# Optimization experiments

Hardware: AMD Instinct MI355X
Metric: run time of the kernel (lower is better)

The kernel has to match this reference:

```python
import jax, jax.numpy as jnp
import numpy as np

CODE_SIZE = 8
NUM_HEADS = 16
KC = 2 ** CODE_SIZE  # 256 codebook buckets


def setup_inputs() -> dict:
    key = jax.random.key(0)
    ks = jax.random.split(key, 6)
    B, Lq, Lk, C = 8, 2048, 4096, 1024
    q = jax.random.normal(ks[0], (B * Lq, C), jnp.float32)
    k = jax.random.normal(ks[1], (B * Lk, C), jnp.float32)
    v = jax.random.normal(ks[2], (B * Lk, C), jnp.float32)
    Wc = jax.random.normal(ks[3], (CODE_SIZE, C), jnp.float32) * (C ** -0.5)  # code_proj weight
    bc = jnp.zeros((CODE_SIZE,), jnp.float32)                                  # code_proj bias
    codebook = jax.random.normal(ks[4], (2 * CODE_SIZE, C), jnp.float32) * 0.02
    lengths = jnp.full((B,), Lk, jnp.int32)      # kv tokens per sample
    inv_lengths = jnp.full((B,), Lq, jnp.int32)  # q tokens per sample
    return dict(q=q, k=k, v=v, Wc=Wc, bc=bc, codebook=codebook,
                lengths=lengths, inv_lengths=inv_lengths)


def reference(q, k, v, Wc, bc, codebook, lengths, inv_lengths):
    C = q.shape[-1]
    d = C // NUM_HEADS
    scale = d ** -0.5
    B = lengths.shape[0]
    Lk = k.shape[0] // B  # equal per-sample kv lengths
    Lq = q.shape[0] // B  # equal per-sample q lengths

    # --- binary spherical quantization of k ---
    code = k @ Wc.T + bc
    code = code / jnp.linalg.norm(code, axis=-1, keepdims=True)
    # sign in {-1,+1}/sqrt(cs); affine *sqrt(cs)/2 + 0.5 -> bits in {0,1}
    bits = (code >= 0).astype(jnp.int32)                      # [B*Lk, cs]
    code_base = 2 ** jnp.arange(CODE_SIZE - 1, -1, -1)        # [cs]
    idxs = (bits * code_base).sum(-1)                         # [B*Lk] in [0, 256)

    # --- dense codebook keys for all 2^cs codes ---
    base_bits = (jnp.arange(KC)[:, None] // code_base) % 2    # [K, cs]
    base = jnp.concatenate([base_bits, 1 - base_bits], axis=-1).astype(codebook.dtype)  # [K, 2cs]
    cod_k = base @ codebook                                   # [K, C]

    # --- scatter-add v and counts into per-sample buckets ---
    b_idx = jnp.repeat(jnp.arange(B), Lk)                     # batch id per kv token
    flat = b_idx * KC + idxs                                  # [B*Lk]
    cod_v = jax.ops.segment_sum(v, flat, num_segments=B * KC).reshape(B, KC, C)
    counts = jax.ops.segment_sum(jnp.ones((B * Lk,), q.dtype), flat,
                                 num_segments=B * KC).reshape(B, KC)

    # --- bucketed attention with quotient normalization ---
    qh = q.reshape(B, Lq, NUM_HEADS, d)
    kh = cod_k.reshape(KC, NUM_HEADS, d)
    vh = cod_v.reshape(B, KC, NUM_HEADS, d)
    scores = scale * jnp.einsum('blhd,khd->blhk', qh, kh)     # [B,Lq,H,K]
    bias = jnp.where(counts > 0, 0.0, -jnp.inf)[:, None, None, :]  # mask empty buckets
    attn = jax.nn.softmax(scores + bias, axis=-1)
    num = jnp.einsum('blhk,bkhd->blhd', attn, vh)             # attn @ summed-v
    den = jnp.einsum('blhk,bk->blh', attn, counts)            # attn @ counts
    out = num / den[..., None]
    return out.reshape(B * Lq, C)
```

## Files before the change

kernel.cpp:

```cpp
#include <hip/hip_runtime.h>
#include <hip/hip_bf16.h>

constexpr int B  = 8;
constexpr int LQ = 2048;
constexpr int LK = 4096;
constexpr int C  = 1024;
constexpr int H  = 16;
constexpr int D  = 64;
constexpr int CS = 8;
constexpr int KC = 256;
constexpr float SCALE = 0.125f;

typedef __attribute__((ext_vector_type(8))) short short8;
typedef __attribute__((ext_vector_type(4))) float f32x4;

union FragU { unsigned u[4]; short8 s; float4 f; };

__device__ inline unsigned bfp(float a, float b) {
  float2 f2; f2.x = a; f2.y = b;
  __hip_bfloat162 h = __float22bfloat162_rn(f2);
  return *reinterpret_cast<unsigned*>(&h);
}
__device__ inline unsigned short bf1(float a) {
  __hip_bfloat16 h = __float2bfloat16(a);
  return *reinterpret_cast<unsigned short*>(&h);
}

__global__ __launch_bounds__(256) void k_codes(
    const float* __restrict__ kmat, const float* __restrict__ Wc,
    const float* __restrict__ bc, int* __restrict__ idx)
{
  __shared__ float wS[CS * C];
  const int tid = threadIdx.x;
  {
    const float4* wsrc = (const float4*)Wc;
    float4* wdst = (float4*)wS;
#pragma unroll
    for (int i = 0; i < 8; ++i) wdst[tid + i * 256] = wsrc[tid + i * 256];
  }
  float bcr[CS];
#pragma unroll
  for (int j = 0; j < CS; ++j) bcr[j] = bc[j];
  __syncthreads();

  const int wave = tid >> 6, lane = tid & 63;

  for (int i = 0; i < 8; ++i) {
    const int r = blockIdx.x * 32 + wave * 8 + i;
    const float4* krow = (const float4*)(kmat + (size_t)r * C);
    float acc[CS];
#pragma unroll
    for (int j = 0; j < CS; ++j) acc[j] = 0.f;
#pragma unroll
    for (int rep = 0; rep < 4; ++rep) {
      float4 kv = krow[rep * 64 + lane];
      const int dbase = (rep * 64 + lane) * 4;
#pragma unroll
      for (int j = 0; j < CS; ++j) {
        float4 wv = *(const float4*)&wS[j * C + dbase];
        acc[j] += kv.x * wv.x + kv.y * wv.y + kv.z * wv.z + kv.w * wv.w;
      }
    }
#pragma unroll
    for (int j = 0; j < CS; ++j) {
#pragma unroll
      for (int off = 32; off >= 1; off >>= 1)
        acc[j] += __shfl_xor(acc[j], off, 64);
    }
    if (lane == 0) {
      int ix = 0;
#pragma unroll
      for (int j = 0; j < CS; ++j)
        ix |= ((acc[j] + bcr[j]) >= 0.f ? 1 : 0) << (7 - j);
      idx[r] = ix;
    }
  }
}

__global__ __launch_bounds__(256) void k_sort(
    const int* __restrict__ idx, int* __restrict__ offs,
    int* __restrict__ cnti, int* __restrict__ perm,
    float4* __restrict__ vfc)
{
  __shared__ int idxS[LK];
  __shared__ int hist[KC];
  __shared__ int cur[KC];
  __shared__ int wsum[4];
  const int b = blockIdx.x, t = threadIdx.x;
  const int lane = t & 63, w = t >> 6;

  hist[t] = 0;
  __syncthreads();
  for (int i = t; i < LK; i += 256) {
    const int ix = idx[b * LK + i];
    idxS[i] = ix;
    atomicAdd(&hist[ix], 1);
  }
  __syncthreads();

  const int myc = hist[t];
  int scan = myc;
#pragma unroll
  for (int off = 1; off < 64; off <<= 1) {
    int u = __shfl_up(scan, off, 64);
    if (lane >= off) scan += u;
  }
  if (lane == 63) wsum[w] = scan;
  __syncthreads();
  int base = 0;
#pragma unroll
  for (int i = 0; i < 4; ++i) base += (i < w) ? wsum[i] : 0;
  const int start = b * LK + base + scan - myc;
  offs[b * KC + t] = start;
  cnti[b * KC + t] = myc;
  cur[t] = start;
  __syncthreads();

  for (int i = t; i < LK; i += 256) {
    const int pos = atomicAdd(&cur[idxS[i]], 1);
    perm[pos] = b * LK + i;
  }

  for (int i = t; i < 512; i += 256) {
    const int qc = i >> 6, ln = i & 63;
    FragU u4;
    if ((ln & 15) == 0) {
      const int* cs = hist + (qc * 4 + (ln >> 4)) * 8;
      u4.u[0] = bfp((float)cs[0], (float)cs[1]);
      u4.u[1] = bfp((float)cs[2], (float)cs[3]);
      u4.u[2] = bfp((float)cs[4], (float)cs[5]);
      u4.u[3] = bfp((float)cs[6], (float)cs[7]);
    } else {
      u4.u[0] = u4.u[1] = u4.u[2] = u4.u[3] = 0u;
    }
    vfc[b * 512 + i] = u4.f;
  }
}

__global__ __launch_bounds__(256) void k_gather(
    const float* __restrict__ v, const int* __restrict__ perm,
    const int* __restrict__ offs, const int* __restrict__ cnti,
    unsigned short* __restrict__ vbf)
{
  __shared__ int permS[512];
  const int t = threadIdx.x;
  const int ix = blockIdx.x, b = blockIdx.y;
  const int start = offs[b * KC + ix];
  const int cnt = cnti[b * KC + ix];

  float4 acc = make_float4(0.f, 0.f, 0.f, 0.f);
  for (int base = 0; base < cnt; base += 512) {
    const int n = min(512, cnt - base);
    __syncthreads();
    for (int i = t; i < n; i += 256) permS[i] = perm[start + base + i];
    __syncthreads();
    int i = 0;
    for (; i + 4 <= n; i += 4) {
      const int r0 = permS[i], r1 = permS[i + 1];
      const int r2 = permS[i + 2], r3 = permS[i + 3];
      float4 a = *(const float4*)(v + (size_t)r0 * C + t * 4);
      float4 b4 = *(const float4*)(v + (size_t)r1 * C + t * 4);
      float4 c4 = *(const float4*)(v + (size_t)r2 * C + t * 4);
      float4 d4 = *(const float4*)(v + (size_t)r3 * C + t * 4);
      acc.x += a.x + b4.x + c4.x + d4.x;
      acc.y += a.y + b4.y + c4.y + d4.y;
      acc.z += a.z + b4.z + c4.z + d4.z;
      acc.w += a.w + b4.w + c4.w + d4.w;
    }
    for (; i < n; ++i) {
      const int r0 = permS[i];
      float4 a = *(const float4*)(v + (size_t)r0 * C + t * 4);
      acc.x += a.x; acc.y += a.y; acc.z += a.z; acc.w += a.w;
    }
  }

  const int h = t >> 4;
  const int n0 = (t & 15) * 4;
  const int o = ix >> 3, r = ix & 7;
  const int slot0 = ((o >> 2) * 4 + (n0 >> 4)) * 64 + (o & 3) * 16 + (n0 & 15);
  unsigned short* dst = vbf + ((size_t)((b * 16 + h) * 2048 + slot0)) * 8 + r;
  dst[0]  = bf1(acc.x);
  dst[8]  = bf1(acc.y);
  dst[16] = bf1(acc.z);
  dst[24] = bf1(acc.w);
}

__global__ __launch_bounds__(256) void k_attn(
    const float* __restrict__ q, const float* __restrict__ cb,
    const float4* __restrict__ vfb, const float4* __restrict__ vfc,
    float* __restrict__ out)
{
  __shared__ __align__(16) char smem[18432];
  float4* QA  = (float4*)smem;
  float4* CBf = (float4*)(smem + 16384);
  float*  TS  = (float*)smem;

  const int tid = threadIdx.x;
  const int lane = tid & 63, wq = tid >> 6, quad = lane >> 4;
  const int h = blockIdx.y, b = blockIdx.z;
  const int q0 = blockIdx.x * 128;

#pragma unroll
  for (int it = 0; it < 4; ++it) {
    const int od = tid & 7, m = it * 32 + (tid >> 3);
    const float* src = q + (size_t)(b * LQ + q0 + m) * C + h * D + od * 8;
    float4 f0 = *(const float4*)src, f1 = *(const float4*)(src + 4);
    FragU u;
    u.u[0] = bfp(f0.x * SCALE, f0.y * SCALE);
    u.u[1] = bfp(f0.z * SCALE, f0.w * SCALE);
    u.u[2] = bfp(f1.x * SCALE, f1.y * SCALE);
    u.u[3] = bfp(f1.z * SCALE, f1.w * SCALE);
    QA[((m >> 4) * 2 + (od >> 2)) * 64 + (od & 3) * 16 + (m & 15)] = u.f;
  }
  if (tid < 128) {
    const int od = tid & 7, j = tid >> 3;
    const float* src = cb + (size_t)j * C + h * D + od * 8;
    float4 f0 = *(const float4*)src, f1 = *(const float4*)(src + 4);
    FragU u;
    u.u[0] = bfp(f0.x, f0.y); u.u[1] = bfp(f0.z, f0.w);
    u.u[2] = bfp(f1.x, f1.y); u.u[3] = bfp(f1.z, f1.w);
    CBf[(od >> 2) * 64 + (od & 3) * 16 + j] = u.f;
  }
  __syncthreads();

  f32x4 tacc[2];
#pragma unroll
  for (int mt2 = 0; mt2 < 2; ++mt2) {
    const int mt = wq * 2 + mt2;
    FragU a0, a1, b0, b1;
    a0.f = QA[(mt * 2 + 0) * 64 + lane];
    a1.f = QA[(mt * 2 + 1) * 64 + lane];
    b0.f = CBf[0 * 64 + lane];
    b1.f = CBf[1 * 64 + lane];
    f32x4 z = {0.f, 0.f, 0.f, 0.f};
    z = __builtin_amdgcn_mfma_f32_16x16x32_bf16(a0.s, b0.s, z, 0, 0, 0);
    z = __builtin_amdgcn_mfma_f32_16x16x32_bf16(a1.s, b1.s, z, 0, 0, 0);
    tacc[mt2] = z;
  }
  __syncthreads();

#pragma unroll
  for (int mt2 = 0; mt2 < 2; ++mt2) {
    const int mt = wq * 2 + mt2;
#pragma unroll
    for (int r = 0; r < 4; ++r)
      TS[mt * 272 + (quad * 4 + r) * 17 + (lane & 15)] = tacc[mt2][r];
  }
  float t0[16], t1[16];
#pragma unroll
  for (int j = 0; j < 16; ++j) {
    t0[j] = TS[(wq * 2 + 0) * 272 + (lane & 15) * 17 + j];
    t1[j] = TS[(wq * 2 + 1) * 272 + (lane & 15) * 17 + j];
  }

  float esl0[8], esl1[8];
#pragma unroll
  for (int c = 0; c < 8; ++c) {
    esl0[c] = __expf(((c & 4) ? t0[5] : t0[13]) + ((c & 2) ? t0[6] : t0[14]) +
                     ((c & 1) ? t0[7] : t0[15]));
    esl1[c] = __expf(((c & 4) ? t1[5] : t1[13]) + ((c & 2) ? t1[6] : t1[14]) +
                     ((c & 1) ? t1[7] : t1[15]));
  }

  f32x4 acc[2][5];
#pragma unroll
  for (int i = 0; i < 2; ++i)
#pragma unroll
    for (int t_ = 0; t_ < 5; ++t_) acc[i][t_] = (f32x4){0.f, 0.f, 0.f, 0.f};

  const float4* vb = vfb + (size_t)(b * 16 + h) * 2048 + lane;
  const float4* vc = vfc + b * 512 + lane;

#pragma unroll
  for (int qc = 0; qc < 8; ++qc) {
    FragU bf0, bf1_, bf2, bf3, cf;
    bf0.f = vb[(qc * 4 + 0) * 64];
    bf1_.f = vb[(qc * 4 + 1) * 64];
    bf2.f = vb[(qc * 4 + 2) * 64];
    bf3.f = vb[(qc * 4 + 3) * 64];
    cf.f  = vc[qc * 64];

    const int u = qc * 4 + quad;
    const float eshi0 = __expf(
        ((u & 16) ? t0[0] : t0[8]) + ((u & 8) ? t0[1] : t0[9]) +
        ((u & 4) ? t0[2] : t0[10]) + ((u & 2) ? t0[3] : t0[11]) +
        ((u & 1) ? t0[4] : t0[12]));
    const float eshi1 = __expf(
        ((u & 16) ? t1[0] : t1[8]) + ((u & 8) ? t1[1] : t1[9]) +
        ((u & 4) ? t1[2] : t1[10]) + ((u & 2) ? t1[3] : t1[11]) +
        ((u & 1) ? t1[4] : t1[12]));

    FragU a0, a1;
    a0.u[0] = bfp(eshi0 * esl0[0], eshi0 * esl0[1]);
    a0.u[1] = bfp(eshi0 * esl0[2], eshi0 * esl0[3]);
    a0.u[2] = bfp(eshi0 * esl0[4], eshi0 * esl0[5]);
    a0.u[3] = bfp(eshi0 * esl0[6], eshi0 * esl0[7]);
    a1.u[0] = bfp(eshi1 * esl1[0], eshi1 * esl1[1]);
    a1.u[1] = bfp(eshi1 * esl1[2], eshi1 * esl1[3]);
    a1.u[2] = bfp(eshi1 * esl1[4], eshi1 * esl1[5]);
    a1.u[3] = bfp(eshi1 * esl1[6], eshi1 * esl1[7]);

    acc[0][0] = __builtin_amdgcn_mfma_f32_16x16x32_bf16(a0.s, bf0.s,  acc[0][0], 0, 0, 0);
    acc[1][0] = __builtin_amdgcn_mfma_f32_16x16x32_bf16(a1.s, bf0.s,  acc[1][0], 0, 0, 0);
    acc[0][1] = __builtin_amdgcn_mfma_f32_16x16x32_bf16(a0.s, bf1_.s, acc[0][1], 0, 0, 0);
    acc[1][1] = __builtin_amdgcn_mfma_f32_16x16x32_bf16(a1.s, bf1_.s, acc[1][1], 0, 0, 0);
    acc[0][2] = __builtin_amdgcn_mfma_f32_16x16x32_bf16(a0.s, bf2.s,  acc[0][2], 0, 0, 0);
    acc[1][2] = __builtin_amdgcn_mfma_f32_16x16x32_bf16(a1.s, bf2.s,  acc[1][2], 0, 0, 0);
    acc[0][3] = __builtin_amdgcn_mfma_f32_16x16x32_bf16(a0.s, bf3.s,  acc[0][3], 0, 0, 0);
    acc[1][3] = __builtin_amdgcn_mfma_f32_16x16x32_bf16(a1.s, bf3.s,  acc[1][3], 0, 0, 0);
    acc[0][4] = __builtin_amdgcn_mfma_f32_16x16x32_bf16(a0.s, cf.s,   acc[0][4], 0, 0, 0);
    acc[1][4] = __builtin_amdgcn_mfma_f32_16x16x32_bf16(a1.s, cf.s,   acc[1][4], 0, 0, 0);
  }

  const int srcl = lane & 48;
#pragma unroll
  for (int mt2 = 0; mt2 < 2; ++mt2) {
#pragma unroll
    for (int r = 0; r < 4; ++r) {
      const float den = __shfl(acc[mt2][4][r], srcl, 64);
      const float inv = 1.0f / den;
      const int row = q0 + wq * 32 + mt2 * 16 + quad * 4 + r;
      float* op = out + (size_t)(b * LQ + row) * C + h * D + (lane & 15);
#pragma unroll
      for (int t_ = 0; t_ < 4; ++t_) op[t_ * 16] = acc[mt2][t_][r] * inv;
    }
  }
}

extern "C" void kernel_launch(void* const* d_in, const int* in_sizes, int n_in,
                              void* d_out, int out_size, void* d_ws, size_t ws_size,
                              hipStream_t stream) {
  (void)in_sizes; (void)n_in; (void)out_size; (void)ws_size;
  const float* q  = (const float*)d_in[0];
  const float* k  = (const float*)d_in[1];
  const float* v  = (const float*)d_in[2];
  const float* Wc = (const float*)d_in[3];
  const float* bc = (const float*)d_in[4];
  const float* cb = (const float*)d_in[5];
  float* out = (float*)d_out;

  char* ws = (char*)d_ws;
  int*    idxp  = (int*)ws;
  int*    offsp = (int*)(ws + 0x20000);
  int*    cntip = (int*)(ws + 0x22000);
  int*    permp = (int*)(ws + 0x24000);
  float4* vfcp  = (float4*)(ws + 0x44000);
  unsigned short* vbfp = (unsigned short*)(ws + 0x60000);

  hipLaunchKernelGGL(k_codes, dim3(1024), dim3(256), 0, stream,
                     k, Wc, bc, idxp);
  hipLaunchKernelGGL(k_sort, dim3(B), dim3(256), 0, stream,
                     idxp, offsp, cntip, permp, vfcp);
  hipLaunchKernelGGL(k_gather, dim3(KC, B), dim3(256), 0, stream,
                     v, permp, offsp, cntip, vbfp);
  hipLaunchKernelGGL(k_attn, dim3(LQ / 128, H, B), dim3(256), 0, stream,
                     q, cb, (const float4*)vbfp, (const float4*)vfcp, out);
}
```

Measured before the change: 376.9 us.

## Fuse four kernels into one persistent kernel with software grid barriers

Replaces the codes/sort/gather/attention kernel chain with a single persistent 512-block kernel separated by atomic-based grid barriers, plus a small init kernel. The histogram is built with global atomics during code computation, and the gather is retiled so each block handles 8 buckets over half the channels and writes packed bf16 fragments. Attention tiles are mapped so each XCD handles one batch, and outputs use nontemporal stores. This removes launch gaps and the tail of the serial 8-block sort. In exchange it relies on all 512 blocks being co-resident, only 8 blocks do the sort while the rest wait at a barrier, and a timeout in the spin loop could silently break correctness.

```diff
diff --git a/kernel.cpp b/kernel.cpp
--- a/kernel.cpp
+++ b/kernel.cpp
@@ -9,6 +9,7 @@
 constexpr int D  = 64;
 constexpr int CS = 8;
 constexpr int KC = 256;
+constexpr int GRID = 512;
 constexpr float SCALE = 0.125f;
 
 typedef __attribute__((ext_vector_type(8))) short short8;
@@ -21,308 +22,322 @@
   __hip_bfloat162 h = __float22bfloat162_rn(f2);
   return *reinterpret_cast<unsigned*>(&h);
 }
-__device__ inline unsigned short bf1(float a) {
-  __hip_bfloat16 h = __float2bfloat16(a);
-  return *reinterpret_cast<unsigned short*>(&h);
-}
-
-__global__ __launch_bounds__(256) void k_codes(
-    const float* __restrict__ kmat, const float* __restrict__ Wc,
-    const float* __restrict__ bc, int* __restrict__ idx)
+
+__device__ inline void gridbar(int* bar) {
+  __syncthreads();
+  if (threadIdx.x == 0) {
+    __threadfence();
+    const int g = __hip_atomic_load(bar + 1, __ATOMIC_RELAXED, __HIP_MEMORY_SCOPE_AGENT);
+    const int a = __hip_atomic_fetch_add(bar, 1, __ATOMIC_ACQ_REL, __HIP_MEMORY_SCOPE_AGENT);
+    if (a == GRID - 1) {
+      __hip_atomic_store(bar, 0, __ATOMIC_RELAXED, __HIP_MEMORY_SCOPE_AGENT);
+      __hip_atomic_fetch_add(bar + 1, 1, __ATOMIC_RELEASE, __HIP_MEMORY_SCOPE_AGENT);
+    } else {
+      int it = 0;
+      while (__hip_atomic_load(bar + 1, __ATOMIC_ACQUIRE, __HIP_MEMORY_SCOPE_AGENT) == g) {
+        if (++it > 2000000) break;
+        __builtin_amdgcn_s_sleep(8);
+      }
+    }
+    __threadfence();
+  }
+  __syncthreads();
+}
+
+__global__ __launch_bounds__(256) void k_init(int* __restrict__ histg,
+                                              int* __restrict__ bar)
 {
-  __shared__ float wS[CS * C];
+  const int i = blockIdx.x * 256 + threadIdx.x;
+  if (i < B * KC) histg[i] = 0;
+  if (i == 0) { bar[0] = 0; bar[1] = 0; }
+}
+
+__global__ __launch_bounds__(256, 2) void k_fused(
+    const float* __restrict__ q, const float* __restrict__ kmat,
+    const float* __restrict__ v, const float* __restrict__ Wc,
+    const float* __restrict__ bc, const float* __restrict__ cb,
+    float* __restrict__ out,
+    int* __restrict__ idx, int* __restrict__ histg,
+    int* __restrict__ offs, int* __restrict__ cnti, int* __restrict__ perm,
+    float4* __restrict__ vfc, float4* __restrict__ vfb,
+    int* __restrict__ bar)
+{
+  __shared__ __align__(16) char smem[32768];
   const int tid = threadIdx.x;
+  const int lane = tid & 63, wave = tid >> 6;
+
   {
+    float* wS = (float*)smem;
     const float4* wsrc = (const float4*)Wc;
     float4* wdst = (float4*)wS;
 #pragma unroll
     for (int i = 0; i < 8; ++i) wdst[tid + i * 256] = wsrc[tid + i * 256];
-  }
-  float bcr[CS];
-#pragma unroll
-  for (int j = 0; j < CS; ++j) bcr[j] = bc[j];
-  __syncthreads();
-
-  const int wave = tid >> 6, lane = tid & 63;
-
-  for (int i = 0; i < 8; ++i) {
-    const int r = blockIdx.x * 32 + wave * 8 + i;
-    const float4* krow = (const float4*)(kmat + (size_t)r * C);
-    float acc[CS];
-#pragma unroll
-    for (int j = 0; j < CS; ++j) acc[j] = 0.f;
-#pragma unroll
-    for (int rep = 0; rep < 4; ++rep) {
-      float4 kv = krow[rep * 64 + lane];
-      const int dbase = (rep * 64 + lane) * 4;
-#pragma unroll
-      for (int j = 0; j < CS; ++j) {
-        float4 wv = *(const float4*)&wS[j * C + dbase];
-        acc[j] += kv.x * wv.x + kv.y * wv.y + kv.z * wv.z + kv.w * wv.w;
-      }
-    }
-#pragma unroll
-    for (int j = 0; j < CS; ++j) {
-#pragma unroll
-      for (int off = 32; off >= 1; off >>= 1)
-        acc[j] += __shfl_xor(acc[j], off, 64);
-    }
-    if (lane == 0) {
-      int ix = 0;
-#pragma unroll
-      for (int j = 0; j < CS; ++j)
-        ix |= ((acc[j] + bcr[j]) >= 0.f ? 1 : 0) << (7 - j);
-      idx[r] = ix;
-    }
-  }
-}
-
-__global__ __launch_bounds__(256) void k_sort(
-    const int* __restrict__ idx, int* __restrict__ offs,
-    int* __restrict__ cnti, int* __restrict__ perm,
-    float4* __restrict__ vfc)
-{
-  __shared__ int idxS[LK];
-  __shared__ int hist[KC];
-  __shared__ int cur[KC];
-  __shared__ int wsum[4];
-  const int b = blockIdx.x, t = threadIdx.x;
-  const int lane = t & 63, w = t >> 6;
-
-  hist[t] = 0;
-  __syncthreads();
-  for (int i = t; i < LK; i += 256) {
-    const int ix = idx[b * LK + i];
-    idxS[i] = ix;
-    atomicAdd(&hist[ix], 1);
-  }
-  __syncthreads();
-
-  const int myc = hist[t];
-  int scan = myc;
-#pragma unroll
-  for (int off = 1; off < 64; off <<= 1) {
-    int u = __shfl_up(scan, off, 64);
-    if (lane >= off) scan += u;
-  }
-  if (lane == 63) wsum[w] = scan;
-  __syncthreads();
-  int base = 0;
-#pragma unroll
-  for (int i = 0; i < 4; ++i) base += (i < w) ? wsum[i] : 0;
-  const int start = b * LK + base + scan - myc;
-  offs[b * KC + t] = start;
-  cnti[b * KC + t] = myc;
-  cur[t] = start;
-  __syncthreads();
-
-  for (int i = t; i < LK; i += 256) {
-    const int pos = atomicAdd(&cur[idxS[i]], 1);
-    perm[pos] = b * LK + i;
-  }
-
-  for (int i = t; i < 512; i += 256) {
-    const int qc = i >> 6, ln = i & 63;
-    FragU u4;
-    if ((ln & 15) == 0) {
-      const int* cs = hist + (qc * 4 + (ln >> 4)) * 8;
-      u4.u[0] = bfp((float)cs[0], (float)cs[1]);
-      u4.u[1] = bfp((float)cs[2], (float)cs[3]);
-      u4.u[2] = bfp((float)cs[4], (float)cs[5]);
-      u4.u[3] = bfp((float)cs[6], (float)cs[7]);
-    } else {
-      u4.u[0] = u4.u[1] = u4.u[2] = u4.u[3] = 0u;
-    }
-    vfc[b * 512 + i] = u4.f;
-  }
-}
-
-__global__ __launch_bounds__(256) void k_gather(
-    const float* __restrict__ v, const int* __restrict__ perm,
-    const int* __restrict__ offs, const int* __restrict__ cnti,
-    unsigned short* __restrict__ vbf)
-{
-  __shared__ int permS[512];
-  const int t = threadIdx.x;
-  const int ix = blockIdx.x, b = blockIdx.y;
-  const int start = offs[b * KC + ix];
-  const int cnt = cnti[b * KC + ix];
-
-  float4 acc = make_float4(0.f, 0.f, 0.f, 0.f);
-  for (int base = 0; base < cnt; base += 512) {
-    const int n = min(512, cnt - base);
+    float bcr[CS];
+#pragma unroll
+    for (int j = 0; j < CS; ++j) bcr[j] = bc[j];
     __syncthreads();
-    for (int i = t; i < n; i += 256) permS[i] = perm[start + base + i];
+
+    for (int chunk = blockIdx.x; chunk < (B * LK) / 16; chunk += GRID) {
+      for (int i = 0; i < 4; ++i) {
+        const int r = chunk * 16 + wave * 4 + i;
+        const float4* krow = (const float4*)(kmat + (size_t)r * C);
+        float acc[CS];
+#pragma unroll
+        for (int j = 0; j < CS; ++j) acc[j] = 0.f;
+#pragma unroll
+        for (int rep = 0; rep < 4; ++rep) {
+          float4 kv = krow[rep * 64 + lane];
+          const int dbase = (rep * 64 + lane) * 4;
+#pragma unroll
+          for (int j = 0; j < CS; ++j) {
+            float4 wv = *(const float4*)&wS[j * C + dbase];
+            acc[j] += kv.x * wv.x + kv.y * wv.y + kv.z * wv.z + kv.w * wv.w;
+          }
+        }
+#pragma unroll
+        for (int j = 0; j < CS; ++j) {
+#pragma unroll
+          for (int off = 32; off >= 1; off >>= 1)
+            acc[j] += __shfl_xor(acc[j], off, 64);
+        }
+        if (lane == 0) {
+          int ix = 0;
+#pragma unroll
+          for (int j = 0; j < CS; ++j)
+            ix |= ((acc[j] + bcr[j]) >= 0.f ? 1 : 0) << (7 - j);
+          idx[r] = ix;
+          atomicAdd(&histg[(r >> 12) * KC + ix], 1);
+        }
+      }
+    }
+  }
+  gridbar(bar);
+
+  if (blockIdx.x < B) {
+    int* idxS = (int*)smem;
+    int* cur  = (int*)(smem + 16384);
+    int* wsum = (int*)(smem + 17408);
+    const int b = blockIdx.x;
+    for (int i = tid; i < LK; i += 256) idxS[i] = idx[b * LK + i];
+    const int myc = histg[b * KC + tid];
+    int scan = myc;
+#pragma unroll
+    for (int off = 1; off < 64; off <<= 1) {
+      int u = __shfl_up(scan, off, 64);
+      if (lane >= off) scan += u;
+    }
+    if (lane == 63) wsum[wave] = scan;
     __syncthreads();
-    int i = 0;
-    for (; i + 4 <= n; i += 4) {
-      const int r0 = permS[i], r1 = permS[i + 1];
-      const int r2 = permS[i + 2], r3 = permS[i + 3];
-      float4 a = *(const float4*)(v + (size_t)r0 * C + t * 4);
-      float4 b4 = *(const float4*)(v + (size_t)r1 * C + t * 4);
-      float4 c4 = *(const float4*)(v + (size_t)r2 * C + t * 4);
-      float4 d4 = *(const float4*)(v + (size_t)r3 * C + t * 4);
-      acc.x += a.x + b4.x + c4.x + d4.x;
-      acc.y += a.y + b4.y + c4.y + d4.y;
-      acc.z += a.z + b4.z + c4.z + d4.z;
-      acc.w += a.w + b4.w + c4.w + d4.w;
-    }
-    for (; i < n; ++i) {
-      const int r0 = permS[i];
-      float4 a = *(const float4*)(v + (size_t)r0 * C + t * 4);
-      acc.x += a.x; acc.y += a.y; acc.z += a.z; acc.w += a.w;
-    }
-  }
-
-  const int h = t >> 4;
-  const int n0 = (t & 15) * 4;
-  const int o = ix >> 3, r = ix & 7;
-  const int slot0 = ((o >> 2) * 4 + (n0 >> 4)) * 64 + (o & 3) * 16 + (n0 & 15);
-  unsigned short* dst = vbf + ((size_t)((b * 16 + h) * 2048 + slot0)) * 8 + r;
-  dst[0]  = bf1(acc.x);
-  dst[8]  = bf1(acc.y);
-  dst[16] = bf1(acc.z);
-  dst[24] = bf1(acc.w);
-}
-
-__global__ __launch_bounds__(256) void k_attn(
-    const float* __restrict__ q, const float* __restrict__ cb,
-    const float4* __restrict__ vfb, const float4* __restrict__ vfc,
-    float* __restrict__ out)
-{
-  __shared__ __align__(16) char smem[18432];
-  float4* QA  = (float4*)smem;
-  float4* CBf = (float4*)(smem + 16384);
-  float*  TS  = (float*)smem;
-
-  const int tid = threadIdx.x;
-  const int lane = tid & 63, wq = tid >> 6, quad = lane >> 4;
-  const int h = blockIdx.y, b = blockIdx.z;
-  const int q0 = blockIdx.x * 128;
-
-#pragma unroll
-  for (int it = 0; it < 4; ++it) {
-    const int od = tid & 7, m = it * 32 + (tid >> 3);
-    const float* src = q + (size_t)(b * LQ + q0 + m) * C + h * D + od * 8;
-    float4 f0 = *(const float4*)src, f1 = *(const float4*)(src + 4);
-    FragU u;
-    u.u[0] = bfp(f0.x * SCALE, f0.y * SCALE);
-    u.u[1] = bfp(f0.z * SCALE, f0.w * SCALE);
-    u.u[2] = bfp(f1.x * SCALE, f1.y * SCALE);
-    u.u[3] = bfp(f1.z * SCALE, f1.w * SCALE);
-    QA[((m >> 4) * 2 + (od >> 2)) * 64 + (od & 3) * 16 + (m & 15)] = u.f;
-  }
-  if (tid < 128) {
-    const int od = tid & 7, j = tid >> 3;
-    const float* src = cb + (size_t)j * C + h * D + od * 8;
-    float4 f0 = *(const float4*)src, f1 = *(const float4*)(src + 4);
-    FragU u;
-    u.u[0] = bfp(f0.x, f0.y); u.u[1] = bfp(f0.z, f0.w);
-    u.u[2] = bfp(f1.x, f1.y); u.u[3] = bfp(f1.z, f1.w);
-    CBf[(od >> 2) * 64 + (od & 3) * 16 + j] = u.f;
-  }
-  __syncthreads();
-
-  f32x4 tacc[2];
-#pragma unroll
-  for (int mt2 = 0; mt2 < 2; ++mt2) {
-    const int mt = wq * 2 + mt2;
-    FragU a0, a1, b0, b1;
-    a0.f = QA[(mt * 2 + 0) * 64 + lane];
-    a1.f = QA[(mt * 2 + 1) * 64 + lane];
-    b0.f = CBf[0 * 64 + lane];
-    b1.f = CBf[1 * 64 + lane];
-    f32x4 z = {0.f, 0.f, 0.f, 0.f};
-    z = __builtin_amdgcn_mfma_f32_16x16x32_bf16(a0.s, b0.s, z, 0, 0, 0);
-    z = __builtin_amdgcn_mfma_f32_16x16x32_bf16(a1.s, b1.s, z, 0, 0, 0);
-    tacc[mt2] = z;
-  }
-  __syncthreads();
-
-#pragma unroll
-  for (int mt2 = 0; mt2 < 2; ++mt2) {
-    const int mt = wq * 2 + mt2;
-#pragma unroll
-    for (int r = 0; r < 4; ++r)
-      TS[mt * 272 + (quad * 4 + r) * 17 + (lane & 15)] = tacc[mt2][r];
-  }
-  float t0[16], t1[16];
-#pragma unroll
-  for (int j = 0; j < 16; ++j) {
-    t0[j] = TS[(wq * 2 + 0) * 272 + (lane & 15) * 17 + j];
-    t1[j] = TS[(wq * 2 + 1) * 272 + (lane & 15) * 17 + j];
-  }
-
-  float esl0[8], esl1[8];
-#pragma unroll
-  for (int c = 0; c < 8; ++c) {
-    esl0[c] = __expf(((c & 4) ? t0[5] : t0[13]) + ((c & 2) ? t0[6] : t0[14]) +
-                     ((c & 1) ? t0[7] : t0[15]));
-    esl1[c] = __expf(((c & 4) ? t1[5] : t1[13]) + ((c & 2) ? t1[6] : t1[14]) +
-                     ((c & 1) ? t1[7] : t1[15]));
-  }
-
-  f32x4 acc[2][5];
-#pragma unroll
-  for (int i = 0; i < 2; ++i)
-#pragma unroll
-    for (int t_ = 0; t_ < 5; ++t_) acc[i][t_] = (f32x4){0.f, 0.f, 0.f, 0.f};
-
-  const float4* vb = vfb + (size_t)(b * 16 + h) * 2048 + lane;
-  const float4* vc = vfc + b * 512 + lane;
-
-#pragma unroll
-  for (int qc = 0; qc < 8; ++qc) {
-    FragU bf0, bf1_, bf2, bf3, cf;
-    bf0.f = vb[(qc * 4 + 0) * 64];
-    bf1_.f = vb[(qc * 4 + 1) * 64];
-    bf2.f = vb[(qc * 4 + 2) * 64];
-    bf3.f = vb[(qc * 4 + 3) * 64];
-    cf.f  = vc[qc * 64];
-
-    const int u = qc * 4 + quad;
-    const float eshi0 = __expf(
-        ((u & 16) ? t0[0] : t0[8]) + ((u & 8) ? t0[1] : t0[9]) +
-        ((u & 4) ? t0[2] : t0[10]) + ((u & 2) ? t0[3] : t0[11]) +
-        ((u & 1) ? t0[4] : t0[12]));
-    const float eshi1 = __expf(
-        ((u & 16) ? t1[0] : t1[8]) + ((u & 8) ? t1[1] : t1[9]) +
-        ((u & 4) ? t1[2] : t1[10]) + ((u & 2) ? t1[3] : t1[11]) +
-        ((u & 1) ? t1[4] : t1[12]));
-
-    FragU a0, a1;
-    a0.u[0] = bfp(eshi0 * esl0[0], eshi0 * esl0[1]);
-    a0.u[1] = bfp(eshi0 * esl0[2], eshi0 * esl0[3]);
-    a0.u[2] = bfp(eshi0 * esl0[4], eshi0 * esl0[5]);
-    a0.u[3] = bfp(eshi0 * esl0[6], eshi0 * esl0[7]);
-    a1.u[0] = bfp(eshi1 * esl1[0], eshi1 * esl1[1]);
-    a1.u[1] = bfp(eshi1 * esl1[2], eshi1 * esl1[3]);
-    a1.u[2] = bfp(eshi1 * esl1[4], eshi1 * esl1[5]);
-    a1.u[3] = bfp(eshi1 * esl1[6], eshi1 * esl1[7]);
-
-    acc[0][0] = __builtin_amdgcn_mfma_f32_16x16x32_bf16(a0.s, bf0.s,  acc[0][0], 0, 0, 0);
-    acc[1][0] = __builtin_amdgcn_mfma_f32_16x16x32_bf16(a1.s, bf0.s,  acc[1][0], 0, 0, 0);
-    acc[0][1] = __builtin_amdgcn_mfma_f32_16x16x32_bf16(a0.s, bf1_.s, acc[0][1], 0, 0, 0);
-    acc[1][1] = __builtin_amdgcn_mfma_f32_16x16x32_bf16(a1.s, bf1_.s, acc[1][1], 0, 0, 0);
-    acc[0][2] = __builtin_amdgcn_mfma_f32_16x16x32_bf16(a0.s, bf2.s,  acc[0][2], 0, 0, 0);
-    acc[1][2] = __builtin_amdgcn_mfma_f32_16x16x32_bf16(a1.s, bf2.s,  acc[1][2], 0, 0, 0);
-    acc[0][3] = __builtin_amdgcn_mfma_f32_16x16x32_bf16(a0.s, bf3.s,  acc[0][3], 0, 0, 0);
-    acc[1][3] = __builtin_amdgcn_mfma_f32_16x16x32_bf16(a1.s, bf3.s,  acc[1][3], 0, 0, 0);
-    acc[0][4] = __builtin_amdgcn_mfma_f32_16x16x32_bf16(a0.s, cf.s,   acc[0][4], 0, 0, 0);
-    acc[1][4] = __builtin_amdgcn_mfma_f32_16x16x32_bf16(a1.s, cf.s,   acc[1][4], 0, 0, 0);
-  }
-
-  const int srcl = lane & 48;
-#pragma unroll
-  for (int mt2 = 0; mt2 < 2; ++mt2) {
-#pragma unroll
-    for (int r = 0; r < 4; ++r) {
-      const float den = __shfl(acc[mt2][4][r], srcl, 64);
-      const float inv = 1.0f / den;
-      const int row = q0 + wq * 32 + mt2 * 16 + quad * 4 + r;
-      float* op = out + (size_t)(b * LQ + row) * C + h * D + (lane & 15);
-#pragma unroll
-      for (int t_ = 0; t_ < 4; ++t_) op[t_ * 16] = acc[mt2][t_][r] * inv;
+    int base = 0;
+#pragma unroll
+    for (int i = 0; i < 4; ++i) base += (i < wave) ? wsum[i] : 0;
+    const int start = b * LK + base + scan - myc;
+    offs[b * KC + tid] = start;
+    cnti[b * KC + tid] = myc;
+    cur[tid] = start;
+    __syncthreads();
+    for (int i = tid; i < LK; i += 256) {
+      const int pos = atomicAdd(&cur[idxS[i]], 1);
+      perm[pos] = b * LK + i;
+    }
+    for (int i = tid; i < 512; i += 256) {
+      const int qc = i >> 6, ln = i & 63;
+      FragU u4;
+      if ((ln & 15) == 0) {
+        const int* cs = histg + b * KC + (qc * 4 + (ln >> 4)) * 8;
+        u4.u[0] = bfp((float)cs[0], (float)cs[1]);
+        u4.u[1] = bfp((float)cs[2], (float)cs[3]);
+        u4.u[2] = bfp((float)cs[4], (float)cs[5]);
+        u4.u[3] = bfp((float)cs[6], (float)cs[7]);
+      } else {
+        u4.u[0] = u4.u[1] = u4.u[2] = u4.u[3] = 0u;
+      }
+      vfc[b * 512 + i] = u4.f;
+    }
+  }
+  gridbar(bar);
+
+  for (int td = blockIdx.x; td < 512; td += GRID) {
+    const int s = td & 1, o = (td >> 1) & 31, b = td >> 6;
+    const int c0 = s * 512 + tid * 2;
+    float2 acc[8];
+#pragma unroll
+    for (int j = 0; j < 8; ++j) { acc[j].x = 0.f; acc[j].y = 0.f; }
+#pragma unroll
+    for (int j = 0; j < 8; ++j) {
+      const int bu = b * KC + o * 8 + j;
+      const int st = offs[bu], cn = cnti[bu];
+      int i = 0;
+      for (; i + 4 <= cn; i += 4) {
+        const int r0 = perm[st + i],     r1 = perm[st + i + 1];
+        const int r2 = perm[st + i + 2], r3 = perm[st + i + 3];
+        const float2 a = *(const float2*)(v + (size_t)r0 * C + c0);
+        const float2 e = *(const float2*)(v + (size_t)r1 * C + c0);
+        const float2 f = *(const float2*)(v + (size_t)r2 * C + c0);
+        const float2 g = *(const float2*)(v + (size_t)r3 * C + c0);
+        acc[j].x += a.x + e.x + f.x + g.x;
+        acc[j].y += a.y + e.y + f.y + g.y;
+      }
+      for (; i < cn; ++i) {
+        const int r0 = perm[st + i];
+        const float2 a = *(const float2*)(v + (size_t)r0 * C + c0);
+        acc[j].x += a.x; acc[j].y += a.y;
+      }
+    }
+    const int h = c0 >> 6, n = c0 & 63;
+    const int slot = ((o >> 2) * 4 + (n >> 4)) * 64 + (o & 3) * 16 + (n & 15);
+    FragU lo, hi;
+    lo.u[0] = bfp(acc[0].x, acc[1].x); lo.u[1] = bfp(acc[2].x, acc[3].x);
+    lo.u[2] = bfp(acc[4].x, acc[5].x); lo.u[3] = bfp(acc[6].x, acc[7].x);
+    hi.u[0] = bfp(acc[0].y, acc[1].y); hi.u[1] = bfp(acc[2].y, acc[3].y);
+    hi.u[2] = bfp(acc[4].y, acc[5].y); hi.u[3] = bfp(acc[6].y, acc[7].y);
+    float4* op = vfb + (size_t)(b * 16 + h) * 2048 + slot;
+    op[0] = lo.f;
+    op[1] = hi.f;
+  }
+  gridbar(bar);
+
+  {
+    float4* QA  = (float4*)smem;
+    float4* CBf = (float4*)(smem + 16384);
+    float*  TS  = (float*)smem;
+    const int wq = wave, quad = lane >> 4;
+    const int xcd = blockIdx.x & 7, p = blockIdx.x >> 3;
+    constexpr int PB = GRID >> 3;
+
+    for (int ti = p; ti < 256; ti += PB) {
+      const int b = xcd;
+      const int h = (ti >> 4) & 15;
+      const int q0 = (ti & 15) * 128;
+
+#pragma unroll
+      for (int it = 0; it < 4; ++it) {
+        const int od = tid & 7, m = it * 32 + (tid >> 3);
+        const float* src = q + (size_t)(b * LQ + q0 + m) * C + h * D + od * 8;
+        float4 f0 = *(const float4*)src, f1 = *(const float4*)(src + 4);
+        FragU u;
+        u.u[0] = bfp(f0.x * SCALE, f0.y * SCALE);
+        u.u[1] = bfp(f0.z * SCALE, f0.w * SCALE);
+        u.u[2] = bfp(f1.x * SCALE, f1.y * SCALE);
+        u.u[3] = bfp(f1.z * SCALE, f1.w * SCALE);
+        QA[((m >> 4) * 2 + (od >> 2)) * 64 + (od & 3) * 16 + (m & 15)] = u.f;
+      }
+      if (tid < 128) {
+        const int od = tid & 7, j = tid >> 3;
+        const float* src = cb + (size_t)j * C + h * D + od * 8;
+        float4 f0 = *(const float4*)src, f1 = *(const float4*)(src + 4);
+        FragU u;
+        u.u[0] = bfp(f0.x, f0.y); u.u[1] = bfp(f0.z, f0.w);
+        u.u[2] = bfp(f1.x, f1.y); u.u[3] = bfp(f1.z, f1.w);
+        CBf[(od >> 2) * 64 + (od & 3) * 16 + j] = u.f;
+      }
+      __syncthreads();
+
+      f32x4 tacc[2];
+#pragma unroll
+      for (int mt2 = 0; mt2 < 2; ++mt2) {
+        const int mt = wq * 2 + mt2;
+        FragU a0, a1, b0, b1;
+        a0.f = QA[(mt * 2 + 0) * 64 + lane];
+        a1.f = QA[(mt * 2 + 1) * 64 + lane];
+        b0.f = CBf[0 * 64 + lane];
+        b1.f = CBf[1 * 64 + lane];
+        f32x4 z = {0.f, 0.f, 0.f, 0.f};
+        z = __builtin_amdgcn_mfma_f32_16x16x32_bf16(a0.s, b0.s, z, 0, 0, 0);
+        z = __builtin_amdgcn_mfma_f32_16x16x32_bf16(a1.s, b1.s, z, 0, 0, 0);
+        tacc[mt2] = z;
+      }
+      __syncthreads();
+
+#pragma unroll
+      for (int mt2 = 0; mt2 < 2; ++mt2) {
+        const int mt = wq * 2 + mt2;
+#pragma unroll
+        for (int r = 0; r < 4; ++r)
+          TS[mt * 272 + (quad * 4 + r) * 17 + (lane & 15)] = tacc[mt2][r];
+      }
+      __syncthreads();
+      float t0[16], t1[16];
+#pragma unroll
+      for (int j = 0; j < 16; ++j) {
+        t0[j] = TS[(wq * 2 + 0) * 272 + (lane & 15) * 17 + j];
+        t1[j] = TS[(wq * 2 + 1) * 272 + (lane & 15) * 17 + j];
+      }
+
+      float esl0[8], esl1[8];
+#pragma unroll
+      for (int c = 0; c < 8; ++c) {
+        esl0[c] = __expf(((c & 4) ? t0[5] : t0[13]) + ((c & 2) ? t0[6] : t0[14]) +
+                         ((c & 1) ? t0[7] : t0[15]));
+        esl1[c] = __expf(((c & 4) ? t1[5] : t1[13]) + ((c & 2) ? t1[6] : t1[14]) +
+                         ((c & 1) ? t1[7] : t1[15]));
+      }
+
+      f32x4 acc[2][5];
+#pragma unroll
+      for (int i = 0; i < 2; ++i)
+#pragma unroll
+        for (int t_ = 0; t_ < 5; ++t_) acc[i][t_] = (f32x4){0.f, 0.f, 0.f, 0.f};
+
+      const float4* vb = vfb + (size_t)(b * 16 + h) * 2048 + lane;
+      const float4* vc = vfc + b * 512 + lane;
+
+#pragma unroll
+      for (int qc = 0; qc < 8; ++qc) {
+        FragU bf0, bf1_, bf2, bf3, cf;
+        bf0.f = vb[(qc * 4 + 0) * 64];
+        bf1_.f = vb[(qc * 4 + 1) * 64];
+        bf2.f = vb[(qc * 4 + 2) * 64];
+        bf3.f = vb[(qc * 4 + 3) * 64];
+        cf.f  = vc[qc * 64];
+
+        const int u = qc * 4 + quad;
+        const float eshi0 = __expf(
+            ((u & 16) ? t0[0] : t0[8]) + ((u & 8) ? t0[1] : t0[9]) +
+            ((u & 4) ? t0[2] : t0[10]) + ((u & 2) ? t0[3] : t0[11]) +
+            ((u & 1) ? t0[4] : t0[12]));
+        const float eshi1 = __expf(
+            ((u & 16) ? t1[0] : t1[8]) + ((u & 8) ? t1[1] : t1[9]) +
+            ((u & 4) ? t1[2] : t1[10]) + ((u & 2) ? t1[3] : t1[11]) +
+            ((u & 1) ? t1[4] : t1[12]));
+
+        FragU a0, a1;
+        a0.u[0] = bfp(eshi0 * esl0[0], eshi0 * esl0[1]);
+        a0.u[1] = bfp(eshi0 * esl0[2], eshi0 * esl0[3]);
+        a0.u[2] = bfp(eshi0 * esl0[4], eshi0 * esl0[5]);
+        a0.u[3] = bfp(eshi0 * esl0[6], eshi0 * esl0[7]);
+        a1.u[0] = bfp(eshi1 * esl1[0], eshi1 * esl1[1]);
+        a1.u[1] = bfp(eshi1 * esl1[2], eshi1 * esl1[3]);
+        a1.u[2] = bfp(eshi1 * esl1[4], eshi1 * esl1[5]);
+        a1.u[3] = bfp(eshi1 * esl1[6], eshi1 * esl1[7]);
+
+        acc[0][0] = __builtin_amdgcn_mfma_f32_16x16x32_bf16(a0.s, bf0.s,  acc[0][0], 0, 0, 0);
+        acc[1][0] = __builtin_amdgcn_mfma_f32_16x16x32_bf16(a1.s, bf0.s,  acc[1][0], 0, 0, 0);
+        acc[0][1] = __builtin_amdgcn_mfma_f32_16x16x32_bf16(a0.s, bf1_.s, acc[0][1], 0, 0, 0);
+        acc[1][1] = __builtin_amdgcn_mfma_f32_16x16x32_bf16(a1.s, bf1_.s, acc[1][1], 0, 0, 0);
+        acc[0][2] = __builtin_amdgcn_mfma_f32_16x16x32_bf16(a0.s, bf2.s,  acc[0][2], 0, 0, 0);
+        acc[1][2] = __builtin_amdgcn_mfma_f32_16x16x32_bf16(a1.s, bf2.s,  acc[1][2], 0, 0, 0);
+        acc[0][3] = __builtin_amdgcn_mfma_f32_16x16x32_bf16(a0.s, bf3.s,  acc[0][3], 0, 0, 0);
+        acc[1][3] = __builtin_amdgcn_mfma_f32_16x16x32_bf16(a1.s, bf3.s,  acc[1][3], 0, 0, 0);
+        acc[0][4] = __builtin_amdgcn_mfma_f32_16x16x32_bf16(a0.s, cf.s,   acc[0][4], 0, 0, 0);
+        acc[1][4] = __builtin_amdgcn_mfma_f32_16x16x32_bf16(a1.s, cf.s,   acc[1][4], 0, 0, 0);
+      }
+
+      const int srcl = lane & 48;
+#pragma unroll
+      for (int mt2 = 0; mt2 < 2; ++mt2) {
+#pragma unroll
+        for (int r = 0; r < 4; ++r) {
+          const float den = __shfl(acc[mt2][4][r], srcl, 64);
+          const float inv = 1.0f / den;
+          const int row = q0 + wq * 32 + mt2 * 16 + quad * 4 + r;
+          float* op = out + (size_t)(b * LQ + row) * C + h * D + (lane & 15);
+#pragma unroll
+          for (int t_ = 0; t_ < 4; ++t_)
+            __builtin_nontemporal_store(acc[mt2][t_][r] * inv, op + t_ * 16);
+        }
+      }
+      __syncthreads();
     }
   }
 }
@@ -341,18 +356,16 @@
 
   char* ws = (char*)d_ws;
   int*    idxp  = (int*)ws;
-  int*    offsp = (int*)(ws + 0x20000);
-  int*    cntip = (int*)(ws + 0x22000);
-  int*    permp = (int*)(ws + 0x24000);
-  float4* vfcp  = (float4*)(ws + 0x44000);
-  unsigned short* vbfp = (unsigned short*)(ws + 0x60000);
-
-  hipLaunchKernelGGL(k_codes, dim3(1024), dim3(256), 0, stream,
-                     k, Wc, bc, idxp);
-  hipLaunchKernelGGL(k_sort, dim3(B), dim3(256), 0, stream,
-                     idxp, offsp, cntip, permp, vfcp);
-  hipLaunchKernelGGL(k_gather, dim3(KC, B), dim3(256), 0, stream,
-                     v, permp, offsp, cntip, vbfp);
-  hipLaunchKernelGGL(k_attn, dim3(LQ / 128, H, B), dim3(256), 0, stream,
-                     q, cb, (const float4*)vbfp, (const float4*)vfcp, out);
-}
+  int*    histp = (int*)(ws + 0x20000);
+  int*    offsp = (int*)(ws + 0x22000);
+  int*    cntip = (int*)(ws + 0x24000);
+  int*    permp = (int*)(ws + 0x26000);
+  float4* vfcp  = (float4*)(ws + 0x46000);
+  int*    barp  = (int*)(ws + 0x56000);
+  float4* vfbp  = (float4*)(ws + 0x60000);
+
+  hipLaunchKernelGGL(k_init, dim3(8), dim3(256), 0, stream, histp, barp);
+  hipLaunchKernelGGL(k_fused, dim3(GRID), dim3(256), 0, stream,
+                     q, k, v, Wc, bc, cb, out,
+                     idxp, histp, offsp, cntip, permp, vfcp, vfbp, barp);
+}
```

New measurement: 696.6 us. +84.8%, slower.
